# Performance work log

Measured on AMD Instinct MI355X. Metric: run time of the kernel, lower is better.

Reference implementation:

```python
import jax, jax.numpy as jnp
import numpy as np

B, N, D = 4, 4096, 256
HEADS, OUT = 4, 64


def setup_inputs() -> dict:
    key = jax.random.key(0)
    ks = jax.random.split(key, 6)
    features = jax.random.normal(ks[0], (B, N, D), dtype=jnp.float32)
    adj = jax.random.randint(ks[1], (B, N, N), 0, 2).astype(jnp.float32)
    s_fc = 1.0 / np.sqrt(D)
    W_fc = jax.random.uniform(ks[2], (OUT * HEADS, D), jnp.float32, -s_fc, s_fc)
    b_fc = jnp.zeros((OUT * HEADS,), jnp.float32)
    s_a = 1.0 / np.sqrt(2 * OUT * HEADS)
    W_attn = jax.random.uniform(ks[3], (HEADS, 2 * OUT * HEADS), jnp.float32, -s_a, s_a)
    b_attn = jax.random.uniform(ks[4], (HEADS,), jnp.float32, -s_a, s_a)
    return {"features": features, "adj": adj, "W_fc": W_fc, "b_fc": b_fc,
            "W_attn": W_attn, "b_attn": b_attn}


def reference(features, adj, W_fc, b_fc, W_attn, b_attn):
    b, n, d = features.shape
    heads = W_attn.shape[0]
    out = W_fc.shape[0] // heads
    # h: [b, n, heads, out]  (fc output reshaped head-major, matching torch .view)
    h = (features @ W_fc.T + b_fc).reshape(b, n, heads, out)
    # attn linear on concat([h_src, h_dst]) flattened as (heads, [src_out | dst_out]),
    # then mean over the `heads` output dim -> score decomposes additively:
    # e[b,i,j] = src[b,j] + dst[b,i] + mean(b_attn)
    Wa = W_attn.reshape(heads, heads, 2 * out)  # [k_out, h_in, 2*out]
    W_src = Wa[:, :, :out].mean(axis=0)   # [heads, out]
    W_dst = Wa[:, :, out:].mean(axis=0)   # [heads, out]
    src = jnp.einsum('bjho,ho->bj', h, W_src)  # depends on source node j
    dst = jnp.einsum('biho,ho->bi', h, W_dst)  # depends on dest node i
    scores = dst[:, :, None] + src[:, None, :] + b_attn.mean()  # [b, n, n]
    scores = scores + (1.0 - adj) * (-1e9)
    alpha = jax.nn.softmax(scores, axis=2)  # softmax over source nodes j
    # torch einsum 'bijk,bjkl->bijl' broadcasts attn's size-1 k against heads,
    # so aggregation uses sum over heads of h; final .mean(dim=2) divides by n.
    h_sum = h.sum(axis=2)  # [b, n, out]
    out_feat = jnp.einsum('bij,bjl->bil', alpha, h_sum) / n
    return out_feat
```

## Files before the change

### kernel.cpp

```cpp
#include <hip/hip_runtime.h>
#include <stdint.h>
#include <math.h>


#define Bz   4
#define Nn   4096
#define Dd   256
#define OUTd 64
#define GTR  80

typedef float    f32x4   __attribute__((ext_vector_type(4)));
typedef __fp16   fp16x2  __attribute__((ext_vector_type(2)));
typedef _Float16 half8_t __attribute__((ext_vector_type(8)));

__device__ inline half8_t cvt8(float4 a, float4 b) {
  union { fp16x2 h2[4]; half8_t h8; } r;
  r.h2[0] = __builtin_amdgcn_cvt_pkrtz(a.x, a.y);
  r.h2[1] = __builtin_amdgcn_cvt_pkrtz(a.z, a.w);
  r.h2[2] = __builtin_amdgcn_cvt_pkrtz(b.x, b.y);
  r.h2[3] = __builtin_amdgcn_cvt_pkrtz(b.z, b.w);
  return r.h8;
}

__global__ __launch_bounds__(256) void k_prep(const float* __restrict__ W_fc,
                                              const float* __restrict__ W_attn,
                                              const float* __restrict__ b_fc,
                                              _Float16* __restrict__ Ut,
                                              float* __restrict__ hb,
                                              float* __restrict__ sb) {
  const int bx = blockIdx.x, t = threadIdx.x;
  if (bx < 64) {
    const int l = bx, d = t;
    float v = W_fc[l * 256 + d] + W_fc[(64 + l) * 256 + d] +
              W_fc[(128 + l) * 256 + d] + W_fc[(192 + l) * 256 + d];
    Ut[l * 256 + d] = (_Float16)v;
    return;
  }
  __shared__ float ws_sh[256];
  {
    const int h = t >> 6, o = t & 63;
    float s = 0.f;
    for (int k = 0; k < 4; ++k) s += W_attn[k * 512 + h * 128 + o];
    ws_sh[t] = s * 0.25f;
  }
  __syncthreads();
  if (bx == 64) {
    const int d = t;
    float v = 0.f;
    for (int ho = 0; ho < 256; ++ho) v += W_fc[ho * 256 + d] * ws_sh[ho];
    Ut[64 * 256 + d] = (_Float16)v;
  } else {
    __shared__ float red[256];
    red[t] = b_fc[t] * ws_sh[t];
    if (t < 64) hb[t] = b_fc[t] + b_fc[64 + t] + b_fc[128 + t] + b_fc[192 + t];
    __syncthreads();
    if (t == 0) {
      float a = 0.f;
      for (int i = 0; i < 256; ++i) a += red[i];
      *sb = a;
    }
  }
}

__global__ __launch_bounds__(256) void k_feat(const float* __restrict__ feat,
                                              const _Float16* __restrict__ Ut,
                                              const float* __restrict__ hb,
                                              const float* __restrict__ sb,
                                              _Float16* __restrict__ Gt) {
  const int b = blockIdx.y;
  const int tid = threadIdx.x;
  const int lane = tid & 63;
  const int wv = tid >> 6;
  const int ln15 = lane & 15;
  const int quad = lane >> 4;
  const int j = blockIdx.x * 64 + wv * 16 + ln15;

  const float* frow = feat + ((size_t)b * Nn + j) * Dd + quad * 8;
  f32x4 acc0 = {0,0,0,0}, acc1 = {0,0,0,0}, acc2 = {0,0,0,0}, acc3 = {0,0,0,0}, acc4 = {0,0,0,0};

  #pragma unroll
  for (int d0 = 0; d0 < Dd; d0 += 32) {
    float4 F0 = *(const float4*)(frow + d0);
    float4 F1 = *(const float4*)(frow + d0 + 4);
    half8_t bf = cvt8(F0, F1);
    const _Float16* up = Ut + (size_t)ln15 * Dd + d0 + quad * 8;
    acc0 = __builtin_amdgcn_mfma_f32_16x16x32_f16(*(const half8_t*)(up + 0 * 16 * Dd), bf, acc0, 0, 0, 0);
    acc1 = __builtin_amdgcn_mfma_f32_16x16x32_f16(*(const half8_t*)(up + 1 * 16 * Dd), bf, acc1, 0, 0, 0);
    acc2 = __builtin_amdgcn_mfma_f32_16x16x32_f16(*(const half8_t*)(up + 2 * 16 * Dd), bf, acc2, 0, 0, 0);
    acc3 = __builtin_amdgcn_mfma_f32_16x16x32_f16(*(const half8_t*)(up + 3 * 16 * Dd), bf, acc3, 0, 0, 0);
    acc4 = __builtin_amdgcn_mfma_f32_16x16x32_f16(*(const half8_t*)(up + 4 * 16 * Dd), bf, acc4, 0, 0, 0);
  }
  float srcv = __shfl(acc4[0], ln15) + sb[0];
  float p = expf(srcv);
  _Float16* gb = Gt + (size_t)b * GTR * Nn;
  #pragma unroll
  for (int r = 0; r < 4; ++r) {
    int lb = quad * 4 + r;
    gb[(size_t)(0  + lb) * Nn + j] = (_Float16)((acc0[r] + hb[0  + lb]) * p);
    gb[(size_t)(16 + lb) * Nn + j] = (_Float16)((acc1[r] + hb[16 + lb]) * p);
    gb[(size_t)(32 + lb) * Nn + j] = (_Float16)((acc2[r] + hb[32 + lb]) * p);
    gb[(size_t)(48 + lb) * Nn + j] = (_Float16)((acc3[r] + hb[48 + lb]) * p);
  }
  if (quad == 0) gb[(size_t)64 * Nn + j] = (_Float16)p;
}

__global__ __launch_bounds__(256) void k_agg(const float* __restrict__ adj,
                                             const _Float16* __restrict__ Gt,
                                             float* __restrict__ out) {
  const int b = blockIdx.y;
  const int tid = threadIdx.x;
  const int lane = tid & 63;
  const int wv = tid >> 6;
  const int ln15 = lane & 15;
  const int quad = lane >> 4;
  const int i0 = blockIdx.x * 64 + wv * 16;

  const float* arow = adj + ((size_t)b * Nn + (i0 + ln15)) * (size_t)Nn + quad * 8;
  const _Float16* g0 = Gt + ((size_t)b * GTR + ln15) * Nn + quad * 8;
  const _Float16* g1 = g0 + (size_t)16 * Nn;
  const _Float16* g2 = g0 + (size_t)32 * Nn;
  const _Float16* g3 = g0 + (size_t)48 * Nn;
  const _Float16* g4 = g0 + (size_t)64 * Nn;

  f32x4 acc0 = {0,0,0,0}, acc1 = {0,0,0,0}, acc2 = {0,0,0,0}, acc3 = {0,0,0,0}, acc4 = {0,0,0,0};

  for (int k0 = 0; k0 < Nn; k0 += 64) {
    float4 A0 = *(const float4*)(arow + k0);
    float4 A1 = *(const float4*)(arow + k0 + 4);
    float4 A2 = *(const float4*)(arow + k0 + 32);
    float4 A3 = *(const float4*)(arow + k0 + 36);
    half8_t b00 = *(const half8_t*)(g0 + k0);
    half8_t b01 = *(const half8_t*)(g1 + k0);
    half8_t b02 = *(const half8_t*)(g2 + k0);
    half8_t b03 = *(const half8_t*)(g3 + k0);
    half8_t b04 = *(const half8_t*)(g4 + k0);
    half8_t b10 = *(const half8_t*)(g0 + k0 + 32);
    half8_t b11 = *(const half8_t*)(g1 + k0 + 32);
    half8_t b12 = *(const half8_t*)(g2 + k0 + 32);
    half8_t b13 = *(const half8_t*)(g3 + k0 + 32);
    half8_t b14 = *(const half8_t*)(g4 + k0 + 32);
    half8_t aF0 = cvt8(A0, A1);
    half8_t aF1 = cvt8(A2, A3);
    acc0 = __builtin_amdgcn_mfma_f32_16x16x32_f16(aF0, b00, acc0, 0, 0, 0);
    acc1 = __builtin_amdgcn_mfma_f32_16x16x32_f16(aF0, b01, acc1, 0, 0, 0);
    acc2 = __builtin_amdgcn_mfma_f32_16x16x32_f16(aF0, b02, acc2, 0, 0, 0);
    acc3 = __builtin_amdgcn_mfma_f32_16x16x32_f16(aF0, b03, acc3, 0, 0, 0);
    acc4 = __builtin_amdgcn_mfma_f32_16x16x32_f16(aF0, b04, acc4, 0, 0, 0);
    acc0 = __builtin_amdgcn_mfma_f32_16x16x32_f16(aF1, b10, acc0, 0, 0, 0);
    acc1 = __builtin_amdgcn_mfma_f32_16x16x32_f16(aF1, b11, acc1, 0, 0, 0);
    acc2 = __builtin_amdgcn_mfma_f32_16x16x32_f16(aF1, b12, acc2, 0, 0, 0);
    acc3 = __builtin_amdgcn_mfma_f32_16x16x32_f16(aF1, b13, acc3, 0, 0, 0);
    acc4 = __builtin_amdgcn_mfma_f32_16x16x32_f16(aF1, b14, acc4, 0, 0, 0);
  }

  float den0 = __shfl(acc4[0], lane & 48);
  float den1 = __shfl(acc4[1], lane & 48);
  float den2 = __shfl(acc4[2], lane & 48);
  float den3 = __shfl(acc4[3], lane & 48);
  const float invn = 1.0f / (float)Nn;
  float* orow = out + ((size_t)b * Nn + i0) * OUTd;
  #pragma unroll
  for (int r = 0; r < 4; ++r) {
    float d = (r == 0) ? den0 : (r == 1) ? den1 : (r == 2) ? den2 : den3;
    float rd = invn / d;
    int ir = quad * 4 + r;
    orow[(size_t)ir * OUTd + 0  + ln15] = acc0[r] * rd;
    orow[(size_t)ir * OUTd + 16 + ln15] = acc1[r] * rd;
    orow[(size_t)ir * OUTd + 32 + ln15] = acc2[r] * rd;
    orow[(size_t)ir * OUTd + 48 + ln15] = acc3[r] * rd;
  }
}

extern "C" void kernel_launch(void* const* d_in, const int* in_sizes, int n_in,
                              void* d_out, int out_size, void* d_ws, size_t ws_size,
                              hipStream_t stream) {
  const float* feat   = (const float*)d_in[0];
  const float* adj    = (const float*)d_in[1];
  const float* W_fc   = (const float*)d_in[2];
  const float* b_fc   = (const float*)d_in[3];
  const float* W_attn = (const float*)d_in[4];
  (void)d_in[5];
  float* out = (float*)d_out;

  char* ws = (char*)d_ws;
  _Float16* Gt = (_Float16*)ws;
  _Float16* Ut = (_Float16*)(ws + 2621440);
  float*    hb  = (float*)(ws + 2621440 + 40960);
  float*    sb  = (float*)(ws + 2621440 + 40960 + 256);

  k_prep<<<66, 256, 0, stream>>>(W_fc, W_attn, b_fc, Ut, hb, sb);
  k_feat<<<dim3(64, 4), 256, 0, stream>>>(feat, Ut, hb, sb, Gt);
  k_agg<<<dim3(64, 4), 256, 0, stream>>>(adj, Gt, out);
}
```

Baseline: 411.6 us.

## Double-buffer adjacency tiles into LDS via async global_load_lds in aggregation

Streams the fp32 adjacency rows for each wave into a per-wave double-buffered LDS region using direct global-to-LDS loads, prefetching the next 128-column tile while the current one feeds MFMAs. It also widens the K step to 128 and issues all Gt loads for the tile before the prefetch. This aims to hide the latency of the dominant 256 MB adj stream and give fully coalesced 512-byte row loads. The trade-offs are a hand-tuned vmcnt wait that depends on instruction ordering, 64 KB of LDS per block limiting occupancy, and an extra LDS read pass.

```diff
diff --git a/kernel.cpp b/kernel.cpp
--- a/kernel.cpp
+++ b/kernel.cpp
@@ -8,6 +8,8 @@
 #define Dd   256
 #define OUTd 64
 #define GTR  80
+#define BKf  128
+#define NTt  (Nn / BKf)
 
 typedef float    f32x4   __attribute__((ext_vector_type(4)));
 typedef __fp16   fp16x2  __attribute__((ext_vector_type(2)));
@@ -20,6 +22,11 @@
   r.h2[2] = __builtin_amdgcn_cvt_pkrtz(b.x, b.y);
   r.h2[3] = __builtin_amdgcn_cvt_pkrtz(b.z, b.w);
   return r.h8;
+}
+
+__device__ inline void gload_lds16(const float* g, float* l) {
+  __builtin_amdgcn_global_load_lds((const __attribute__((address_space(1))) void*)g,
+                                   (__attribute__((address_space(3))) void*)l, 16, 0, 0);
 }
 
 __global__ __launch_bounds__(256) void k_prep(const float* __restrict__ W_fc,
@@ -107,6 +114,7 @@
 __global__ __launch_bounds__(256) void k_agg(const float* __restrict__ adj,
                                              const _Float16* __restrict__ Gt,
                                              float* __restrict__ out) {
+  __shared__ float lds[16384];
   const int b = blockIdx.y;
   const int tid = threadIdx.x;
   const int lane = tid & 63;
@@ -115,7 +123,9 @@
   const int quad = lane >> 4;
   const int i0 = blockIdx.x * 64 + wv * 16;
 
-  const float* arow = adj + ((size_t)b * Nn + (i0 + ln15)) * (size_t)Nn + quad * 8;
+  const float* gstage = adj + ((size_t)b * Nn + (i0 + (lane >> 5))) * (size_t)Nn + (lane & 31) * 4;
+  float* ldsw = &lds[wv * 4096];
+
   const _Float16* g0 = Gt + ((size_t)b * GTR + ln15) * Nn + quad * 8;
   const _Float16* g1 = g0 + (size_t)16 * Nn;
   const _Float16* g2 = g0 + (size_t)32 * Nn;
@@ -124,33 +134,46 @@
 
   f32x4 acc0 = {0,0,0,0}, acc1 = {0,0,0,0}, acc2 = {0,0,0,0}, acc3 = {0,0,0,0}, acc4 = {0,0,0,0};
 
-  for (int k0 = 0; k0 < Nn; k0 += 64) {
-    float4 A0 = *(const float4*)(arow + k0);
-    float4 A1 = *(const float4*)(arow + k0 + 4);
-    float4 A2 = *(const float4*)(arow + k0 + 32);
-    float4 A3 = *(const float4*)(arow + k0 + 36);
-    half8_t b00 = *(const half8_t*)(g0 + k0);
-    half8_t b01 = *(const half8_t*)(g1 + k0);
-    half8_t b02 = *(const half8_t*)(g2 + k0);
-    half8_t b03 = *(const half8_t*)(g3 + k0);
-    half8_t b04 = *(const half8_t*)(g4 + k0);
-    half8_t b10 = *(const half8_t*)(g0 + k0 + 32);
-    half8_t b11 = *(const half8_t*)(g1 + k0 + 32);
-    half8_t b12 = *(const half8_t*)(g2 + k0 + 32);
-    half8_t b13 = *(const half8_t*)(g3 + k0 + 32);
-    half8_t b14 = *(const half8_t*)(g4 + k0 + 32);
-    half8_t aF0 = cvt8(A0, A1);
-    half8_t aF1 = cvt8(A2, A3);
-    acc0 = __builtin_amdgcn_mfma_f32_16x16x32_f16(aF0, b00, acc0, 0, 0, 0);
-    acc1 = __builtin_amdgcn_mfma_f32_16x16x32_f16(aF0, b01, acc1, 0, 0, 0);
-    acc2 = __builtin_amdgcn_mfma_f32_16x16x32_f16(aF0, b02, acc2, 0, 0, 0);
-    acc3 = __builtin_amdgcn_mfma_f32_16x16x32_f16(aF0, b03, acc3, 0, 0, 0);
-    acc4 = __builtin_amdgcn_mfma_f32_16x16x32_f16(aF0, b04, acc4, 0, 0, 0);
-    acc0 = __builtin_amdgcn_mfma_f32_16x16x32_f16(aF1, b10, acc0, 0, 0, 0);
-    acc1 = __builtin_amdgcn_mfma_f32_16x16x32_f16(aF1, b11, acc1, 0, 0, 0);
-    acc2 = __builtin_amdgcn_mfma_f32_16x16x32_f16(aF1, b12, acc2, 0, 0, 0);
-    acc3 = __builtin_amdgcn_mfma_f32_16x16x32_f16(aF1, b13, acc3, 0, 0, 0);
-    acc4 = __builtin_amdgcn_mfma_f32_16x16x32_f16(aF1, b14, acc4, 0, 0, 0);
+  #pragma unroll
+  for (int m = 0; m < 8; ++m)
+    gload_lds16(gstage + (size_t)(m * 2) * Nn, ldsw + m * 256);
+
+  for (int t = 0; t < NTt; ++t) {
+    const int k0 = t * BKf;
+    const int cb = t & 1;
+    const int nb = cb ^ 1;
+
+    half8_t bg0[4], bg1[4], bg2[4], bg3[4], bg4[4];
+    #pragma unroll
+    for (int s = 0; s < 4; ++s) {
+      const int kk = k0 + s * 32;
+      bg0[s] = *(const half8_t*)(g0 + kk);
+      bg1[s] = *(const half8_t*)(g1 + kk);
+      bg2[s] = *(const half8_t*)(g2 + kk);
+      bg3[s] = *(const half8_t*)(g3 + kk);
+      bg4[s] = *(const half8_t*)(g4 + kk);
+    }
+    __builtin_amdgcn_sched_barrier(0);
+
+    const int kn = (t + 1 < NTt) ? (t + 1) * BKf : 0;
+    #pragma unroll
+    for (int m = 0; m < 8; ++m)
+      gload_lds16(gstage + (size_t)(m * 2) * Nn + kn, ldsw + nb * 2048 + m * 256);
+
+    asm volatile("s_waitcnt vmcnt(28)" ::: "memory");
+
+    const float* lb = ldsw + cb * 2048 + ln15 * 128;
+    #pragma unroll
+    for (int s = 0; s < 4; ++s) {
+      float4 A0 = *(const float4*)(lb + s * 32 + quad * 8);
+      float4 A1 = *(const float4*)(lb + s * 32 + quad * 8 + 4);
+      half8_t aF = cvt8(A0, A1);
+      acc0 = __builtin_amdgcn_mfma_f32_16x16x32_f16(aF, bg0[s], acc0, 0, 0, 0);
+      acc1 = __builtin_amdgcn_mfma_f32_16x16x32_f16(aF, bg1[s], acc1, 0, 0, 0);
+      acc2 = __builtin_amdgcn_mfma_f32_16x16x32_f16(aF, bg2[s], acc2, 0, 0, 0);
+      acc3 = __builtin_amdgcn_mfma_f32_16x16x32_f16(aF, bg3[s], acc3, 0, 0, 0);
+      acc4 = __builtin_amdgcn_mfma_f32_16x16x32_f16(aF, bg4[s], acc4, 0, 0, 0);
+    }
   }
 
   float den0 = __shfl(acc4[0], lane & 48);
```

Result: no change. 411.7 us (+0.0%).
